# Optimization experiments

Measured on AMD Instinct MI355X. Metric: run time of the kernel, lower is better.

## Reference

```python
import jax, jax.numpy as jnp
import numpy as np

V, E, H, ENC, ATT = 10000, 256, 512, 512, 512
B, S, NF, MAXLEN = 128, 25, 196, 64


def setup_inputs() -> dict:
    key = jax.random.key(0)
    ks = jax.random.split(key, 24)
    g = lambda k, shp: (jax.random.normal(k, shp, dtype=jnp.float32) * 0.05)
    emb = g(ks[0], (V, E)).at[0].set(0.0)  # padding_idx=0 row zeroed
    return {
        'decoder_input': jax.random.randint(ks[1], (B, S), 0, V, dtype=jnp.int32),
        'encoder_outputs': jax.random.normal(ks[2], (B, NF, ENC), dtype=jnp.float32),
        'emb': emb,
        'pos_emb': g(ks[3], (MAXLEN, E)),
        'Uw': g(ks[4], (ATT, ENC)), 'Ub': g(ks[5], (ATT,)),
        'Ww': g(ks[6], (ATT, H)), 'Wb': g(ks[7], (ATT,)),
        'Aw': g(ks[8], (1, ATT)), 'Ab': g(ks[9], (1,)),
        'init_h_w': g(ks[10], (H, ENC)), 'init_h_b': g(ks[11], (H,)),
        'init_c_w': g(ks[12], (H, ENC)), 'init_c_b': g(ks[13], (H,)),
        'W_ih': g(ks[14], (4 * H, E + ENC)), 'W_hh': g(ks[15], (4 * H, H)),
        'b_ih': g(ks[16], (4 * H,)), 'b_hh': g(ks[17], (4 * H,)),
        'fcn_w': g(ks[18], (V, H)), 'fcn_b': g(ks[19], (V,)),
    }


def reference(decoder_input, encoder_outputs, emb, pos_emb, Uw, Ub, Ww, Wb, Aw, Ab,
              init_h_w, init_h_b, init_c_w, init_c_b, W_ih, W_hh, b_ih, b_hh,
              fcn_w, fcn_b):
    # Loop-invariant attention key projection: U(features) -> [B, NF, ATT]
    u_hs = jnp.einsum('bne,ae->bna', encoder_outputs, Uw) + Ub
    mean_enc = encoder_outputs.mean(axis=1)                  # [B, ENC]
    h0 = mean_enc @ init_h_w.T + init_h_b                    # [B, H]
    c0 = mean_enc @ init_c_w.T + init_c_b
    tokens = decoder_input.T                                 # [S, B]
    positions = jnp.arange(tokens.shape[0])

    def step(carry, inp):
        h, c = carry
        tok, pos = inp
        embeds = emb[tok] + pos_emb[pos]                     # [B, E]
        w_ah = h @ Ww.T + Wb                                 # [B, ATT]
        scores = jnp.tanh(u_hs + w_ah[:, None, :]) @ Aw[0] + Ab[0]  # [B, NF]
        alpha = jax.nn.softmax(scores, axis=1)
        context = jnp.einsum('bnd,bn->bd', encoder_outputs, alpha)  # [B, ENC]
        x = jnp.concatenate([embeds, context], axis=1)       # [B, E+ENC]
        gates = x @ W_ih.T + b_ih + h @ W_hh.T + b_hh        # [B, 4H]
        i, f, g_, o = jnp.split(gates, 4, axis=1)
        c_new = jax.nn.sigmoid(f) * c + jax.nn.sigmoid(i) * jnp.tanh(g_)
        h_new = jax.nn.sigmoid(o) * jnp.tanh(c_new)
        out = h_new @ fcn_w.T + fcn_b                        # [B, V] (dropout=eval identity)
        return (h_new, c_new), (out, alpha)

    _, (outs, alphas) = jax.lax.scan(step, (h0, c0), (tokens, positions))
    return outs.transpose(1, 0, 2), alphas.transpose(1, 0, 2)
```

## Files before the change

kernel.cpp:

```cpp
#include <hip/hip_runtime.h>

constexpr int B_ = 128, S_ = 25, NF_ = 196, ENC_ = 512, ATT_ = 512;
constexpr int H_ = 512, E_ = 256, V_ = 10000, G4_ = 2048;
constexpr int VPAD_ = 10112;

typedef __attribute__((ext_vector_type(8))) __bf16 bf16x8;
typedef __attribute__((ext_vector_type(4))) __bf16 bf16x4;
typedef __attribute__((ext_vector_type(4))) float f32x4;

__device__ __forceinline__ float bflo(unsigned u) {
    return __builtin_bit_cast(float, u << 16);
}
__device__ __forceinline__ float bfhi(unsigned u) {
    return __builtin_bit_cast(float, u & 0xffff0000u);
}
__device__ __forceinline__ float fast_tanhf(float x) {
    float e = __expf(2.f * x);
    return 1.f - 2.f * __fdividef(1.f, e + 1.f);
}
__device__ __forceinline__ float fast_sigf(float x) {
    return __fdividef(1.f, 1.f + __expf(-x));
}

__device__ __forceinline__ int gperm(int n) {
    int j = (n & 15) + ((n >> 6) << 4);
    int g = (n >> 4) & 3;
    return g * 512 + j;
}

__device__ __forceinline__ void gload16(const __bf16* src, __bf16* dst) {
    __builtin_amdgcn_global_load_lds(
        (const __attribute__((address_space(1))) unsigned*)src,
        (__attribute__((address_space(3))) unsigned*)dst, 16, 0, 0);
}

__global__ __launch_bounds__(256) void k_setup(
    const float* __restrict__ enc, __bf16* __restrict__ enc_bf,
    const float* __restrict__ Uw, __bf16* __restrict__ Uw_bf,
    const float* __restrict__ Ww, unsigned* __restrict__ W2,
    const float* __restrict__ W_ih, __bf16* __restrict__ WihE_r,
    const float* __restrict__ W_hh, __bf16* __restrict__ Wcat,
    const float* __restrict__ b_ih, const float* __restrict__ b_hh,
    float* __restrict__ bsum_r,
    const int* __restrict__ dec, const float* __restrict__ emb,
    const float* __restrict__ pose, __bf16* __restrict__ embeds_bf,
    const float* __restrict__ fcw, __bf16* __restrict__ fcw_bf) {
    __shared__ float Ts[32][65];
    int bid = blockIdx.x, t = threadIdx.x;

    if (bid < 12544) {
        int i = bid * 256 + t;
        if (i < 3211264) {
            float4 v = *(const float4*)&enc[(size_t)i * 4];
            bf16x4 o;
            o[0] = (__bf16)v.x; o[1] = (__bf16)v.y; o[2] = (__bf16)v.z; o[3] = (__bf16)v.w;
            *(bf16x4*)&enc_bf[(size_t)i * 4] = o;
        }
    } else if (bid < 12800) {
        int i = (bid - 12544) * 256 + t;
        float4 v = *(const float4*)&Uw[(size_t)i * 4];
        bf16x4 o;
        o[0] = (__bf16)v.x; o[1] = (__bf16)v.y; o[2] = (__bf16)v.z; o[3] = (__bf16)v.w;
        *(bf16x4*)&Uw_bf[(size_t)i * 4] = o;
    } else if (bid < 12928) {
        int l = bid - 12800;
        int k0 = (l & 15) * 32, j0 = (l >> 4) * 64;
        int c = t & 31, rr = t >> 5;
#pragma unroll
        for (int i = 0; i < 8; ++i) {
            int j = j0 + rr + i * 8;
            Ts[c][rr + i * 8] = Ww[(size_t)j * 512 + k0 + c];
        }
        __syncthreads();
#pragma unroll
        for (int i = 0; i < 4; ++i) {
            int kr = (t >> 5) + i * 8;
            int jc = t & 31;
            __bf16 b0 = (__bf16)Ts[kr][2 * jc], b1 = (__bf16)Ts[kr][2 * jc + 1];
            unsigned u = (unsigned)__builtin_bit_cast(unsigned short, b0)
                       | ((unsigned)__builtin_bit_cast(unsigned short, b1) << 16);
            W2[(size_t)(k0 + kr) * 256 + (j0 >> 1) + jc] = u;
        }
    } else if (bid < 14976) {
        int n = bid - 12928;
        int row = gperm(n);
        WihE_r[(size_t)n * 256 + t] = (__bf16)W_ih[(size_t)row * 768 + t];
    } else if (bid < 17024) {
        int n = bid - 14976;
        int row = gperm(n);
#pragma unroll
        for (int i = 0; i < 4; ++i) {
            int k = t + i * 256;
            float v = (k < 512) ? W_ih[(size_t)row * 768 + 256 + k]
                                : W_hh[(size_t)row * 512 + (k - 512)];
            Wcat[(size_t)n * 1024 + k] = (__bf16)v;
        }
    } else if (bid < 17032) {
        int n = (bid - 17024) * 256 + t;
        int row = gperm(n);
        bsum_r[n] = b_ih[row] + b_hh[row];
    } else if (bid < 20232) {
        int bx = bid - 17032;
        int s = bx >> 7, b = bx & 127;
        int tok = dec[b * S_ + s];
        embeds_bf[(size_t)bx * E_ + t] = (__bf16)(emb[tok * E_ + t] + pose[s * E_ + t]);
    } else {
        int i = (bid - 20232) * 256 + t;
        if (i < VPAD_ * 512 / 4) {
            int e = i * 4;
            int row = e >> 9;
            bf16x4 o;
            if (row < V_) {
                float4 v = *(const float4*)&fcw[(size_t)row * 512 + (e & 511)];
                o[0] = (__bf16)v.x; o[1] = (__bf16)v.y; o[2] = (__bf16)v.z; o[3] = (__bf16)v.w;
            } else {
                o[0] = o[1] = o[2] = o[3] = (__bf16)0.f;
            }
            *(bf16x4*)&fcw_bf[(size_t)e] = o;
        }
    }
}

__global__ __launch_bounds__(1024) void k_init2(const float* __restrict__ enc,
                                                const float* __restrict__ ihw, const float* __restrict__ ihb,
                                                const float* __restrict__ icw, const float* __restrict__ icb,
                                                __bf16* __restrict__ Abuf0, float* __restrict__ cbuf) {
    __shared__ float pm[1024];
    __shared__ __align__(16) float mean[512];
    int b = blockIdx.x, t = threadIdx.x;
    int d = t & 511, q = t >> 9;
    const float* ep = enc + ((size_t)b * 196 + q * 98) * 512 + d;
    float sum = 0.f;
#pragma unroll 7
    for (int n = 0; n < 98; ++n) sum += ep[(size_t)n * 512];
    pm[t] = sum;
    __syncthreads();
    if (t < 512) mean[t] = (pm[t] + pm[t + 512]) * (1.f / 196.f);
    __syncthreads();
    int w = t >> 6, ln = t & 63;
    float4 m4a = *(const float4*)&mean[ln * 8];
    float4 m4b = *(const float4*)&mean[ln * 8 + 4];
#pragma unroll 4
    for (int i = 0; i < 32; ++i) {
        int j = i * 16 + w;
        const float4* wh = (const float4*)&ihw[(size_t)j * 512 + ln * 8];
        const float4* wc = (const float4*)&icw[(size_t)j * 512 + ln * 8];
        float4 ha = wh[0], hb = wh[1], ca = wc[0], cb = wc[1];
        float ah = m4a.x * ha.x + m4a.y * ha.y + m4a.z * ha.z + m4a.w * ha.w
                 + m4b.x * hb.x + m4b.y * hb.y + m4b.z * hb.z + m4b.w * hb.w;
        float ac = m4a.x * ca.x + m4a.y * ca.y + m4a.z * ca.z + m4a.w * ca.w
                 + m4b.x * cb.x + m4b.y * cb.y + m4b.z * cb.z + m4b.w * cb.w;
#pragma unroll
        for (int off = 32; off; off >>= 1) {
            ah += __shfl_xor(ah, off);
            ac += __shfl_xor(ac, off);
        }
        if (ln == 0) {
            Abuf0[(size_t)b * 1024 + 512 + j] = (__bf16)(ah + ihb[j]);
            cbuf[b * 512 + j] = ac + icb[j];
        }
    }
}

__global__ __launch_bounds__(256) void k_gemms(
    const __bf16* __restrict__ Aa, const __bf16* __restrict__ Ba,
    const float* __restrict__ ba, __bf16* __restrict__ Ca,
    const __bf16* __restrict__ Ab, const __bf16* __restrict__ Bb,
    const float* __restrict__ bb, __bf16* __restrict__ Cb) {
    __shared__ __align__(16) __bf16 As[128 * 64];
    __shared__ __align__(16) __bf16 Bs[128 * 64];
    int bid = blockIdx.x, tid = threadIdx.x;
    const __bf16 *A, *Bm;
    const float* bias;
    __bf16* C;
    int lda, K, ldc, m0, n0;
    if (bid < 784) {
        A = Aa; Bm = Ba; bias = ba; C = Ca; lda = 512; K = 512; ldc = 512;
        m0 = (bid % 196) * 128; n0 = (bid / 196) * 128;
    } else {
        int i = bid - 784;
        A = Ab; Bm = Bb; bias = bb; C = Cb; lda = 256; K = 256; ldc = 2048;
        m0 = (i % 25) * 128; n0 = (i / 25) * 128;
    }
    int lane = tid & 63, w = tid >> 6;
    int wm = (w & 1) * 64, wn = (w >> 1) * 64;
    f32x4 acc[4][4] = {};
    int lrow = lane >> 3;
    int kgd = lane & 7;

    for (int k0 = 0; k0 < K; k0 += 64) {
#pragma unroll
        for (int i = 0; i < 4; ++i) {
            int row = w * 32 + i * 8 + lrow;
            int kgs = kgd ^ (row & 7);
            gload16(A + (size_t)(m0 + row) * lda + k0 + kgs * 8, &As[row * 64 + kgd * 8]);
            gload16(Bm + (size_t)(n0 + row) * K + k0 + kgs * 8, &Bs[row * 64 + kgd * 8]);
        }
        __syncthreads();
        bf16x8 af[4][2], bfr[4][2];
#pragma unroll
        for (int f = 0; f < 4; ++f) {
#pragma unroll
            for (int ks = 0; ks < 2; ++ks) {
                int ra = wm + f * 16 + (lane & 15);
                int rb = wn + f * 16 + (lane & 15);
                int kgl = ks * 4 + (lane >> 4);
                af[f][ks]  = *(const bf16x8*)&As[ra * 64 + (kgl ^ (ra & 7)) * 8];
                bfr[f][ks] = *(const bf16x8*)&Bs[rb * 64 + (kgl ^ (rb & 7)) * 8];
            }
        }
#pragma unroll
        for (int fm = 0; fm < 4; ++fm)
#pragma unroll
            for (int fn = 0; fn < 4; ++fn)
#pragma unroll
                for (int ks = 0; ks < 2; ++ks)
                    acc[fm][fn] = __builtin_amdgcn_mfma_f32_16x16x32_bf16(
                        af[fm][ks], bfr[fn][ks], acc[fm][fn], 0, 0, 0);
        __syncthreads();
    }
    int cm = (lane >> 4) * 4, cn = lane & 15;
#pragma unroll
    for (int fm = 0; fm < 4; ++fm)
#pragma unroll
        for (int fn = 0; fn < 4; ++fn)
#pragma unroll
            for (int r = 0; r < 4; ++r) {
                int gm = m0 + wm + fm * 16 + cm + r;
                int gn = n0 + wn + fn * 16 + cn;
                C[(size_t)gm * ldc + gn] = (__bf16)(acc[fm][fn][r] + bias[gn]);
            }
}

__global__ __launch_bounds__(256) void k_fcn(
    const __bf16* __restrict__ A, const __bf16* __restrict__ Bm,
    const float* __restrict__ bias1, float* __restrict__ Cout) {
    __shared__ __align__(16) __bf16 As[128 * 64];
    __shared__ __align__(16) __bf16 Bs[128 * 64];
    int tid = threadIdx.x;
    int lane = tid & 63, w = tid >> 6;
    int nwg = gridDim.x * gridDim.y;
    int bid = blockIdx.y * gridDim.x + blockIdx.x;
    int q = nwg >> 3, r0 = nwg & 7;
    int xcd = bid & 7, lid = bid >> 3;
    int wgid = (xcd < r0) ? xcd * (q + 1) + lid : r0 * (q + 1) + (xcd - r0) * q + lid;
    int m0 = (wgid % gridDim.x) * 128;
    int n0 = (wgid / gridDim.x) * 128;

    int wm = (w & 1) * 64, wn = (w >> 1) * 64;
    f32x4 acc[4][4] = {};
    int lrow = lane >> 3;
    int kgd = lane & 7;

    for (int k0 = 0; k0 < 512; k0 += 64) {
#pragma unroll
        for (int i = 0; i < 4; ++i) {
            int row = w * 32 + i * 8 + lrow;
            int kgs = kgd ^ (row & 7);
            gload16(A + (size_t)(m0 + row) * 512 + k0 + kgs * 8, &As[row * 64 + kgd * 8]);
            gload16(Bm + (size_t)(n0 + row) * 512 + k0 + kgs * 8, &Bs[row * 64 + kgd * 8]);
        }
        __syncthreads();
        bf16x8 af[4][2], bfr[4][2];
#pragma unroll
        for (int f = 0; f < 4; ++f) {
#pragma unroll
            for (int ks = 0; ks < 2; ++ks) {
                int ra = wm + f * 16 + (lane & 15);
                int rb = wn + f * 16 + (lane & 15);
                int kgl = ks * 4 + (lane >> 4);
                af[f][ks]  = *(const bf16x8*)&As[ra * 64 + (kgl ^ (ra & 7)) * 8];
                bfr[f][ks] = *(const bf16x8*)&Bs[rb * 64 + (kgl ^ (rb & 7)) * 8];
            }
        }
#pragma unroll
        for (int fm = 0; fm < 4; ++fm)
#pragma unroll
            for (int fn = 0; fn < 4; ++fn)
#pragma unroll
                for (int ks = 0; ks < 2; ++ks)
                    acc[fm][fn] = __builtin_amdgcn_mfma_f32_16x16x32_bf16(
                        af[fm][ks], bfr[fn][ks], acc[fm][fn], 0, 0, 0);
        __syncthreads();
    }
    int cm = (lane >> 4) * 4, cn = lane & 15;
#pragma unroll
    for (int fm = 0; fm < 4; ++fm) {
#pragma unroll
        for (int fn = 0; fn < 4; ++fn) {
#pragma unroll
            for (int r = 0; r < 4; ++r) {
                int gm = m0 + wm + fm * 16 + cm + r;
                int gn = n0 + wn + fn * 16 + cn;
                if (gn < V_) {
                    int orow = (gm & 127) * S_ + (gm >> 7);
                    Cout[(size_t)orow * V_ + gn] = acc[fm][fn][r] + bias1[gn];
                }
            }
        }
    }
}

__global__ __launch_bounds__(1024) void k_attn2(
    const __bf16* __restrict__ u_hs,
    const unsigned* __restrict__ enc2,
    const unsigned* __restrict__ W2,
    const float* __restrict__ Wb, const float* __restrict__ Aw,
    __bf16* __restrict__ Abuf,
    float* __restrict__ alphas, int s) {
    __shared__ __align__(16) float hs[512];
    __shared__ float wah[512];
    __shared__ float pc[2048];
    __shared__ float sc[200];
    int b = blockIdx.x, t = threadIdx.x;
    int ln = t & 63, w = t >> 6;

    if (t < 256) {
        unsigned u = ((const unsigned*)Abuf)[b * 512 + 256 + t];
        hs[2 * t] = bflo(u); hs[2 * t + 1] = bfhi(u);
    }
    __syncthreads();
    {
        int jp = t & 255, kq = t >> 8;
        float a0 = 0.f, a1 = 0.f;
        const unsigned* wp = W2 + (size_t)(kq * 128) * 256 + jp;
        const float4* h4 = (const float4*)(hs + kq * 128);
#pragma unroll 4
        for (int k4 = 0; k4 < 32; ++k4) {
            float4 hk = h4[k4];
            unsigned w0 = wp[(k4 * 4 + 0) * 256];
            unsigned w1 = wp[(k4 * 4 + 1) * 256];
            unsigned w2 = wp[(k4 * 4 + 2) * 256];
            unsigned w3 = wp[(k4 * 4 + 3) * 256];
            a0 += hk.x * bflo(w0); a1 += hk.x * bfhi(w0);
            a0 += hk.y * bflo(w1); a1 += hk.y * bfhi(w1);
            a0 += hk.z * bflo(w2); a1 += hk.z * bfhi(w2);
            a0 += hk.w * bflo(w3); a1 += hk.w * bfhi(w3);
        }
        pc[kq * 512 + 2 * jp] = a0;
        pc[kq * 512 + 2 * jp + 1] = a1;
    }
    __syncthreads();
    if (t < 512)
        wah[t] = pc[t] + pc[512 + t] + pc[1024 + t] + pc[1536 + t] + Wb[t];
    __syncthreads();
    {
        float av[8], wv[8];
#pragma unroll
        for (int i = 0; i < 8; ++i) { av[i] = Aw[ln * 8 + i]; wv[i] = wah[ln * 8 + i]; }
        for (int n = w; n < NF_; n += 16) {
            bf16x8 u8 = *(const bf16x8*)(u_hs + ((size_t)(b * NF_ + n)) * 512 + ln * 8);
            float acc = 0.f;
#pragma unroll
            for (int i = 0; i < 8; ++i)
                acc += fast_tanhf((float)u8[i] + wv[i]) * av[i];
#pragma unroll
            for (int off = 32; off; off >>= 1) acc += __shfl_xor(acc, off);
            if (ln == 0) sc[n] = __expf(acc);
        }
    }
    __syncthreads();
    float sum = sc[ln] + sc[ln + 64] + sc[ln + 128];
    if (ln < 4) sum += sc[ln + 192];
#pragma unroll
    for (int off = 32; off; off >>= 1) sum += __shfl_xor(sum, off);
    float inv = __fdividef(1.f, sum);
    if (t < NF_) alphas[((size_t)b * S_ + s) * NF_ + t] = sc[t] * inv;
    {
        int p2 = t & 255, q2 = t >> 8;
        float c0 = 0.f, c1 = 0.f;
        for (int i = q2; i < NF_; i += 4) {
            unsigned u = enc2[((size_t)(b * NF_ + i)) * 256 + p2];
            float a = sc[i];
            c0 += a * bflo(u); c1 += a * bfhi(u);
        }
        pc[q2 * 512 + 2 * p2] = c0;
        pc[q2 * 512 + 2 * p2 + 1] = c1;
    }
    __syncthreads();
    if (t < 512)
        Abuf[(size_t)b * 1024 + t] =
            (__bf16)((pc[t] + pc[512 + t] + pc[1024 + t] + pc[1536 + t]) * inv);
}

__global__ __launch_bounds__(256) void k_gates(
    const __bf16* __restrict__ Abuf,
    const __bf16* __restrict__ Wcat,
    const __bf16* __restrict__ gatespre,
    float* __restrict__ cbuf,
    __bf16* __restrict__ AbufN,
    __bf16* __restrict__ Hall_bf,
    int s) {
    __shared__ __align__(16) __bf16 As[2][16 * 64];
    __shared__ __align__(16) __bf16 Bs[2][64 * 64];
    __shared__ float Red[1024];
    __shared__ float Gs[16][68];
    int t = threadIdx.x;
    int lane = t & 63, w = t >> 6;
    int m0 = blockIdx.x * 16, n0 = blockIdx.y * 64;
    int kh = w >> 1, nh = w & 1;
    f32x4 acc[2] = {};
    int ah = t >> 7;
    int arow = (t & 127) >> 3;
    int ake = (t & 7) * 8;
    int akg = t & 7;
    int srow = t >> 3;
    int ke = (t & 7) * 8;
    int kgw = t & 7;

    for (int k0 = 0; k0 < 512; k0 += 64) {
        {
            int kb = ah * 512 + k0;
            bf16x8 av = *(const bf16x8*)(Abuf + (size_t)(m0 + arow) * 1024 + kb + ake);
            *(bf16x8*)&As[ah][arow * 64 + (akg ^ (arow & 7)) * 8] = av;
        }
#pragma unroll
        for (int h = 0; h < 2; ++h) {
            int kb = h * 512 + k0;
#pragma unroll
            for (int it = 0; it < 2; ++it) {
                int row = it * 32 + srow;
                bf16x8 bv = *(const bf16x8*)(Wcat + (size_t)(n0 + row) * 1024 + kb + ke);
                *(bf16x8*)&Bs[h][row * 64 + (kgw ^ (row & 7)) * 8] = bv;
            }
        }
        __syncthreads();
        bf16x8 af[2], bfr[2][2];
#pragma unroll
        for (int ks = 0; ks < 2; ++ks) {
            int ra = lane & 15;
            int kgl = ks * 4 + (lane >> 4);
            af[ks] = *(const bf16x8*)&As[kh][ra * 64 + ((kgl ^ (ra & 7))) * 8];
#pragma unroll
            for (int fn = 0; fn < 2; ++fn) {
                int rb = nh * 32 + fn * 16 + (lane & 15);
                bfr[fn][ks] = *(const bf16x8*)&Bs[kh][rb * 64 + ((kgl ^ (rb & 7))) * 8];
            }
        }
#pragma unroll
        for (int fn = 0; fn < 2; ++fn)
#pragma unroll
            for (int ks = 0; ks < 2; ++ks)
                acc[fn] = __builtin_amdgcn_mfma_f32_16x16x32_bf16(
                    af[ks], bfr[fn][ks], acc[fn], 0, 0, 0);
        __syncthreads();
    }
    int base = (nh * 64 + lane) * 8;
    if (kh == 1) {
#pragma unroll
        for (int fn = 0; fn < 2; ++fn)
#pragma unroll
            for (int r = 0; r < 4; ++r) Red[base + fn * 4 + r] = acc[fn][r];
    }
    __syncthreads();
    if (kh == 0) {
        int cm = (lane >> 4) * 4, cn = lane & 15;
#pragma unroll
        for (int fn = 0; fn < 2; ++fn)
#pragma unroll
            for (int r = 0; r < 4; ++r)
                Gs[cm + r][nh * 32 + fn * 16 + cn] = acc[fn][r] + Red[base + fn * 4 + r];
    }
    __syncthreads();
    {
        int row = t >> 4, jlo = t & 15;
        int b = m0 + row;
        int j = (n0 >> 6) * 16 + jlo;
        const __bf16* gp = gatespre + ((size_t)(s * B_ + b)) * G4_ + n0 + jlo;
        float qi = Gs[row][jlo]      + (float)gp[0];
        float qf = Gs[row][16 + jlo] + (float)gp[16];
        float qg = Gs[row][32 + jlo] + (float)gp[32];
        float qo = Gs[row][48 + jlo] + (float)gp[48];
        float ig = fast_sigf(qi), fg = fast_sigf(qf);
        float gg = fast_tanhf(qg), og = fast_sigf(qo);
        int ci = b * 512 + j;
        float cnew = fg * cbuf[ci] + ig * gg;
        float hn = og * fast_tanhf(cnew);
        cbuf[ci] = cnew;
        __bf16 hb = (__bf16)hn;
        AbufN[(size_t)b * 1024 + 512 + j] = hb;
        Hall_bf[(size_t)(s + 1) * 65536 + ci] = hb;
    }
}

extern "C" void kernel_launch(void* const* d_in, const int* in_sizes, int n_in,
                              void* d_out, int out_size, void* d_ws, size_t ws_size,
                              hipStream_t stream) {
    const int*   dec  = (const int*)d_in[0];
    const float* enc  = (const float*)d_in[1];
    const float* emb  = (const float*)d_in[2];
    const float* pose = (const float*)d_in[3];
    const float* Uw   = (const float*)d_in[4];
    const float* Ub   = (const float*)d_in[5];
    const float* Ww   = (const float*)d_in[6];
    const float* Wb   = (const float*)d_in[7];
    const float* Aw   = (const float*)d_in[8];
    const float* ihw  = (const float*)d_in[10];
    const float* ihb  = (const float*)d_in[11];
    const float* icw  = (const float*)d_in[12];
    const float* icb  = (const float*)d_in[13];
    const float* W_ih = (const float*)d_in[14];
    const float* W_hh = (const float*)d_in[15];
    const float* b_ih = (const float*)d_in[16];
    const float* b_hh = (const float*)d_in[17];
    const float* fcw  = (const float*)d_in[18];
    const float* fcb  = (const float*)d_in[19];
    float* out = (float*)d_out;
    char*  wsb = (char*)d_ws;

    size_t o = 0;
    __bf16*   enc_bf   = (__bf16*)(wsb + o); o += (size_t)25088 * 512 * 2;
    __bf16*   u_hs_bf  = (__bf16*)(wsb + o); o += (size_t)25088 * 512 * 2;
    __bf16*   gpre_bf  = (__bf16*)(wsb + o); o += (size_t)3200 * 2048 * 2;
    __bf16*   Hall_bf  = (__bf16*)(wsb + o); o += (size_t)26 * 65536 * 2;
    float*    cbuf     = (float*)(wsb + o);  o += (size_t)65536 * 4;
    __bf16*   Abuf     = (__bf16*)(wsb + o); o += (size_t)2 * 128 * 1024 * 2;
    __bf16*   Uw_bf    = (__bf16*)(wsb + o); o += (size_t)262144 * 2;
    unsigned* W2       = (unsigned*)(wsb + o); o += (size_t)512 * 256 * 4;
    __bf16*   WihE_r   = (__bf16*)(wsb + o); o += (size_t)2048 * 256 * 2;
    __bf16*   embeds_bf= (__bf16*)(wsb + o); o += (size_t)3200 * 256 * 2;
    __bf16*   Wcat     = (__bf16*)(wsb + o); o += (size_t)2048 * 1024 * 2;
    float*    bsum_r   = (float*)(wsb + o);  o += (size_t)2048 * 4;
    __bf16*   fcw_bf   = (__bf16*)(wsb + o); o += (size_t)VPAD_ * 512 * 2;

    k_setup<<<25288, 256, 0, stream>>>(enc, enc_bf, Uw, Uw_bf, Ww, W2,
                                       W_ih, WihE_r, W_hh, Wcat,
                                       b_ih, b_hh, bsum_r,
                                       dec, emb, pose, embeds_bf, fcw, fcw_bf);
    k_init2<<<B_, 1024, 0, stream>>>(enc, ihw, ihb, icw, icb, Abuf, cbuf);
    k_gemms<<<1184, 256, 0, stream>>>(enc_bf, Uw_bf, Ub, u_hs_bf,
                                      embeds_bf, WihE_r, bsum_r, gpre_bf);

    for (int s = 0; s < S_; ++s) {
        __bf16* Ap = Abuf + (size_t)(s & 1) * 131072;
        __bf16* An = Abuf + (size_t)((s + 1) & 1) * 131072;
        k_attn2<<<B_, 1024, 0, stream>>>(u_hs_bf, (const unsigned*)enc_bf, W2, Wb, Aw,
                                         Ap, out + 32000000, s);
        k_gates<<<dim3(8, 32), 256, 0, stream>>>(Ap, Wcat, gpre_bf, cbuf, An, Hall_bf, s);
    }

    k_fcn<<<dim3(25, 79), 256, 0, stream>>>(Hall_bf + 65536, fcw_bf, fcb, out);
}
```

Before: 1.335 ms.

## Split attention over feature halves and move softmax normalization into gates kernel

The per-step attention kernel now runs on a 128x2 grid of 512-thread blocks. Each block handles half of the 196 features and writes unnormalized context partials, exp-score sums and raw exp scores to workspace. The gates kernel combines the two halves, normalizes by the summed denominator while loading its A tile, and writes the alphas. This gives the attention step twice as many blocks to spread across CUs, but each block now recomputes the full W·h projection and extra global traffic passes between the kernels.

```diff
diff --git a/kernel.cpp b/kernel.cpp
--- a/kernel.cpp
+++ b/kernel.cpp
@@ -301,18 +301,20 @@
     }
 }
 
-__global__ __launch_bounds__(1024) void k_attn2(
+__global__ __launch_bounds__(512) void k_attn3(
     const __bf16* __restrict__ u_hs,
     const unsigned* __restrict__ enc2,
     const unsigned* __restrict__ W2,
     const float* __restrict__ Wb, const float* __restrict__ Aw,
-    __bf16* __restrict__ Abuf,
-    float* __restrict__ alphas, int s) {
+    const __bf16* __restrict__ Abuf,
+    float* __restrict__ pctx,
+    float* __restrict__ lpart,
+    float* __restrict__ esg) {
     __shared__ __align__(16) float hs[512];
     __shared__ float wah[512];
-    __shared__ float pc[2048];
-    __shared__ float sc[200];
-    int b = blockIdx.x, t = threadIdx.x;
+    __shared__ float pc[1024];
+    __shared__ float es[100];
+    int b = blockIdx.x, hh = blockIdx.y, t = threadIdx.x;
     int ln = t & 63, w = t >> 6;
 
     if (t < 256) {
@@ -321,12 +323,12 @@
     }
     __syncthreads();
     {
-        int jp = t & 255, kq = t >> 8;
+        int jp = t & 255, q = t >> 8;
         float a0 = 0.f, a1 = 0.f;
-        const unsigned* wp = W2 + (size_t)(kq * 128) * 256 + jp;
-        const float4* h4 = (const float4*)(hs + kq * 128);
+        const unsigned* wp = W2 + (size_t)(q * 256) * 256 + jp;
+        const float4* h4 = (const float4*)(hs + q * 256);
 #pragma unroll 4
-        for (int k4 = 0; k4 < 32; ++k4) {
+        for (int k4 = 0; k4 < 64; ++k4) {
             float4 hk = h4[k4];
             unsigned w0 = wp[(k4 * 4 + 0) * 256];
             unsigned w1 = wp[(k4 * 4 + 1) * 256];
@@ -337,18 +339,18 @@
             a0 += hk.z * bflo(w2); a1 += hk.z * bfhi(w2);
             a0 += hk.w * bflo(w3); a1 += hk.w * bfhi(w3);
         }
-        pc[kq * 512 + 2 * jp] = a0;
-        pc[kq * 512 + 2 * jp + 1] = a1;
-    }
-    __syncthreads();
-    if (t < 512)
-        wah[t] = pc[t] + pc[512 + t] + pc[1024 + t] + pc[1536 + t] + Wb[t];
+        pc[q * 512 + 2 * jp] = a0;
+        pc[q * 512 + 2 * jp + 1] = a1;
+    }
+    __syncthreads();
+    wah[t] = pc[t] + pc[512 + t] + Wb[t];
     __syncthreads();
     {
         float av[8], wv[8];
 #pragma unroll
         for (int i = 0; i < 8; ++i) { av[i] = Aw[ln * 8 + i]; wv[i] = wah[ln * 8 + i]; }
-        for (int n = w; n < NF_; n += 16) {
+        for (int nl = w; nl < 98; nl += 8) {
+            int n = hh * 98 + nl;
             bf16x8 u8 = *(const bf16x8*)(u_hs + ((size_t)(b * NF_ + n)) * 512 + ln * 8);
             float acc = 0.f;
 #pragma unroll
@@ -356,31 +358,30 @@
                 acc += fast_tanhf((float)u8[i] + wv[i]) * av[i];
 #pragma unroll
             for (int off = 32; off; off >>= 1) acc += __shfl_xor(acc, off);
-            if (ln == 0) sc[n] = __expf(acc);
-        }
-    }
-    __syncthreads();
-    float sum = sc[ln] + sc[ln + 64] + sc[ln + 128];
-    if (ln < 4) sum += sc[ln + 192];
-#pragma unroll
-    for (int off = 32; off; off >>= 1) sum += __shfl_xor(sum, off);
-    float inv = __fdividef(1.f, sum);
-    if (t < NF_) alphas[((size_t)b * S_ + s) * NF_ + t] = sc[t] * inv;
+            if (ln == 0) es[nl] = __expf(acc);
+        }
+    }
+    __syncthreads();
     {
         int p2 = t & 255, q2 = t >> 8;
         float c0 = 0.f, c1 = 0.f;
-        for (int i = q2; i < NF_; i += 4) {
-            unsigned u = enc2[((size_t)(b * NF_ + i)) * 256 + p2];
-            float a = sc[i];
+        for (int i = q2; i < 98; i += 2) {
+            unsigned u = enc2[((size_t)(b * NF_ + hh * 98 + i)) * 256 + p2];
+            float a = es[i];
             c0 += a * bflo(u); c1 += a * bfhi(u);
         }
         pc[q2 * 512 + 2 * p2] = c0;
         pc[q2 * 512 + 2 * p2 + 1] = c1;
     }
     __syncthreads();
-    if (t < 512)
-        Abuf[(size_t)b * 1024 + t] =
-            (__bf16)((pc[t] + pc[512 + t] + pc[1024 + t] + pc[1536 + t]) * inv);
+    pctx[((size_t)(hh * 128 + b)) * 512 + t] = pc[t] + pc[512 + t];
+    if (t < 98) esg[b * 256 + hh * 98 + t] = es[t];
+    if (t < 64) {
+        float v = es[t] + ((t + 64 < 98) ? es[t + 64] : 0.f);
+#pragma unroll
+        for (int off = 32; off; off >>= 1) v += __shfl_xor(v, off);
+        if (t == 0) lpart[hh * 128 + b] = v;
+    }
 }
 
 __global__ __launch_bounds__(256) void k_gates(
@@ -390,7 +391,8 @@
     float* __restrict__ cbuf,
     __bf16* __restrict__ AbufN,
     __bf16* __restrict__ Hall_bf,
-    int s) {
+    const float* __restrict__ pctx, const float* __restrict__ lpart,
+    const float* __restrict__ esg, float* __restrict__ alphas, int s) {
     __shared__ __align__(16) __bf16 As[2][16 * 64];
     __shared__ __align__(16) __bf16 Bs[2][64 * 64];
     __shared__ float Red[1024];
@@ -408,11 +410,35 @@
     int ke = (t & 7) * 8;
     int kgw = t & 7;
 
+    if (blockIdx.y == 0) {
+        for (int qq = t; qq < 16 * 196; qq += 256) {
+            int row = qq / 196, n = qq - row * 196;
+            float inv = __fdividef(1.f, lpart[m0 + row] + lpart[128 + m0 + row]);
+            alphas[((size_t)(m0 + row) * S_ + s) * NF_ + n] =
+                esg[(m0 + row) * 256 + n] * inv;
+        }
+    }
+
     for (int k0 = 0; k0 < 512; k0 += 64) {
-        {
-            int kb = ah * 512 + k0;
-            bf16x8 av = *(const bf16x8*)(Abuf + (size_t)(m0 + arow) * 1024 + kb + ake);
-            *(bf16x8*)&As[ah][arow * 64 + (akg ^ (arow & 7)) * 8] = av;
+        if (ah == 0) {
+            const float* p0 = pctx + (size_t)(m0 + arow) * 512 + k0 + ake;
+            const float* p1 = p0 + 128 * 512;
+            float inv = __fdividef(1.f, lpart[m0 + arow] + lpart[128 + m0 + arow]);
+            float4 a0v = *(const float4*)p0, a1v = *(const float4*)(p0 + 4);
+            float4 b0v = *(const float4*)p1, b1v = *(const float4*)(p1 + 4);
+            bf16x8 v;
+            v[0] = (__bf16)((a0v.x + b0v.x) * inv);
+            v[1] = (__bf16)((a0v.y + b0v.y) * inv);
+            v[2] = (__bf16)((a0v.z + b0v.z) * inv);
+            v[3] = (__bf16)((a0v.w + b0v.w) * inv);
+            v[4] = (__bf16)((a1v.x + b1v.x) * inv);
+            v[5] = (__bf16)((a1v.y + b1v.y) * inv);
+            v[6] = (__bf16)((a1v.z + b1v.z) * inv);
+            v[7] = (__bf16)((a1v.w + b1v.w) * inv);
+            *(bf16x8*)&As[0][arow * 64 + (akg ^ (arow & 7)) * 8] = v;
+        } else {
+            bf16x8 av = *(const bf16x8*)(Abuf + (size_t)(m0 + arow) * 1024 + 512 + k0 + ake);
+            *(bf16x8*)&As[1][arow * 64 + (akg ^ (arow & 7)) * 8] = av;
         }
 #pragma unroll
         for (int h = 0; h < 2; ++h) {
@@ -522,6 +548,9 @@
     __bf16*   Wcat     = (__bf16*)(wsb + o); o += (size_t)2048 * 1024 * 2;
     float*    bsum_r   = (float*)(wsb + o);  o += (size_t)2048 * 4;
     __bf16*   fcw_bf   = (__bf16*)(wsb + o); o += (size_t)VPAD_ * 512 * 2;
+    float*    pctx     = (float*)(wsb + o);  o += (size_t)2 * 128 * 512 * 4;
+    float*    lpart    = (float*)(wsb + o);  o += (size_t)256 * 4;
+    float*    esg      = (float*)(wsb + o);  o += (size_t)128 * 256 * 4;
 
     k_setup<<<25288, 256, 0, stream>>>(enc, enc_bf, Uw, Uw_bf, Ww, W2,
                                        W_ih, WihE_r, W_hh, Wcat,
@@ -534,9 +563,10 @@
     for (int s = 0; s < S_; ++s) {
         __bf16* Ap = Abuf + (size_t)(s & 1) * 131072;
         __bf16* An = Abuf + (size_t)((s + 1) & 1) * 131072;
-        k_attn2<<<B_, 1024, 0, stream>>>(u_hs_bf, (const unsigned*)enc_bf, W2, Wb, Aw,
-                                         Ap, out + 32000000, s);
-        k_gates<<<dim3(8, 32), 256, 0, stream>>>(Ap, Wcat, gpre_bf, cbuf, An, Hall_bf, s);
+        k_attn3<<<dim3(B_, 2), 512, 0, stream>>>(u_hs_bf, (const unsigned*)enc_bf, W2,
+                                                 Wb, Aw, Ap, pctx, lpart, esg);
+        k_gates<<<dim3(8, 32), 256, 0, stream>>>(Ap, Wcat, gpre_bf, cbuf, An, Hall_bf,
+                                                 pctx, lpart, esg, out + 32000000, s);
     }
 
     k_fcn<<<dim3(25, 79), 256, 0, stream>>>(Hall_bf + 65536, fcw_bf, fcb, out);
```

Result: slower. 1.383 ms (+3.6%).

## Fuse attention and gate kernels per step using flag-based inter-block sync

Applied to the files above, without the earlier changes.

Merges the per-step attention kernel and the LSTM gate GEMM kernel into one launch of 384 blocks. The first 128 blocks compute attention per batch row and publish a per-row flag with release semantics. The remaining blocks spin on the flags for their 16-row slab before running the gate MFMA GEMM. This removes one kernel launch and its boundary per step (25 fewer launches) and lets gate tiles start as soon as their rows are ready. The risks are deadlock if the spinning blocks get scheduled ahead of the attention blocks and occupy the resources they need, and wasted occupancy because the gate blocks launch with 1024 threads but use only 256.

```diff
diff --git a/kernel.cpp b/kernel.cpp
--- a/kernel.cpp
+++ b/kernel.cpp
@@ -44,7 +44,8 @@
     float* __restrict__ bsum_r,
     const int* __restrict__ dec, const float* __restrict__ emb,
     const float* __restrict__ pose, __bf16* __restrict__ embeds_bf,
-    const float* __restrict__ fcw, __bf16* __restrict__ fcw_bf) {
+    const float* __restrict__ fcw, __bf16* __restrict__ fcw_bf,
+    int* __restrict__ flag) {
     __shared__ float Ts[32][65];
     int bid = blockIdx.x, t = threadIdx.x;
 
@@ -104,7 +105,7 @@
         int s = bx >> 7, b = bx & 127;
         int tok = dec[b * S_ + s];
         embeds_bf[(size_t)bx * E_ + t] = (__bf16)(emb[tok * E_ + t] + pose[s * E_ + t]);
-    } else {
+    } else if (bid < 25288) {
         int i = (bid - 20232) * 256 + t;
         if (i < VPAD_ * 512 / 4) {
             int e = i * 4;
@@ -118,6 +119,8 @@
             }
             *(bf16x4*)&fcw_bf[(size_t)e] = o;
         }
+    } else {
+        if (t < 128) flag[t] = 0;
     }
 }
 
@@ -301,185 +304,199 @@
     }
 }
 
-__global__ __launch_bounds__(1024) void k_attn2(
-    const __bf16* __restrict__ u_hs,
-    const unsigned* __restrict__ enc2,
-    const unsigned* __restrict__ W2,
-    const float* __restrict__ Wb, const float* __restrict__ Aw,
-    __bf16* __restrict__ Abuf,
-    float* __restrict__ alphas, int s) {
+__global__ __launch_bounds__(1024) void k_step(
+    const __bf16* __restrict__ u_hs, const unsigned* __restrict__ enc2,
+    const unsigned* __restrict__ W2, const float* __restrict__ Wb,
+    const float* __restrict__ Aw, const __bf16* __restrict__ Wcat,
+    const __bf16* __restrict__ gatespre, float* __restrict__ cbuf,
+    __bf16* __restrict__ Abuf, __bf16* __restrict__ AbufN,
+    __bf16* __restrict__ Hall_bf, float* __restrict__ alphas,
+    int* __restrict__ flag, int s) {
     __shared__ __align__(16) float hs[512];
     __shared__ float wah[512];
     __shared__ float pc[2048];
     __shared__ float sc[200];
-    int b = blockIdx.x, t = threadIdx.x;
-    int ln = t & 63, w = t >> 6;
-
-    if (t < 256) {
-        unsigned u = ((const unsigned*)Abuf)[b * 512 + 256 + t];
-        hs[2 * t] = bflo(u); hs[2 * t + 1] = bfhi(u);
-    }
-    __syncthreads();
-    {
-        int jp = t & 255, kq = t >> 8;
-        float a0 = 0.f, a1 = 0.f;
-        const unsigned* wp = W2 + (size_t)(kq * 128) * 256 + jp;
-        const float4* h4 = (const float4*)(hs + kq * 128);
-#pragma unroll 4
-        for (int k4 = 0; k4 < 32; ++k4) {
-            float4 hk = h4[k4];
-            unsigned w0 = wp[(k4 * 4 + 0) * 256];
-            unsigned w1 = wp[(k4 * 4 + 1) * 256];
-            unsigned w2 = wp[(k4 * 4 + 2) * 256];
-            unsigned w3 = wp[(k4 * 4 + 3) * 256];
-            a0 += hk.x * bflo(w0); a1 += hk.x * bfhi(w0);
-            a0 += hk.y * bflo(w1); a1 += hk.y * bfhi(w1);
-            a0 += hk.z * bflo(w2); a1 += hk.z * bfhi(w2);
-            a0 += hk.w * bflo(w3); a1 += hk.w * bfhi(w3);
-        }
-        pc[kq * 512 + 2 * jp] = a0;
-        pc[kq * 512 + 2 * jp + 1] = a1;
-    }
-    __syncthreads();
-    if (t < 512)
-        wah[t] = pc[t] + pc[512 + t] + pc[1024 + t] + pc[1536 + t] + Wb[t];
-    __syncthreads();
-    {
-        float av[8], wv[8];
-#pragma unroll
-        for (int i = 0; i < 8; ++i) { av[i] = Aw[ln * 8 + i]; wv[i] = wah[ln * 8 + i]; }
-        for (int n = w; n < NF_; n += 16) {
-            bf16x8 u8 = *(const bf16x8*)(u_hs + ((size_t)(b * NF_ + n)) * 512 + ln * 8);
-            float acc = 0.f;
-#pragma unroll
-            for (int i = 0; i < 8; ++i)
-                acc += fast_tanhf((float)u8[i] + wv[i]) * av[i];
-#pragma unroll
-            for (int off = 32; off; off >>= 1) acc += __shfl_xor(acc, off);
-            if (ln == 0) sc[n] = __expf(acc);
-        }
-    }
-    __syncthreads();
-    float sum = sc[ln] + sc[ln + 64] + sc[ln + 128];
-    if (ln < 4) sum += sc[ln + 192];
-#pragma unroll
-    for (int off = 32; off; off >>= 1) sum += __shfl_xor(sum, off);
-    float inv = __fdividef(1.f, sum);
-    if (t < NF_) alphas[((size_t)b * S_ + s) * NF_ + t] = sc[t] * inv;
-    {
-        int p2 = t & 255, q2 = t >> 8;
-        float c0 = 0.f, c1 = 0.f;
-        for (int i = q2; i < NF_; i += 4) {
-            unsigned u = enc2[((size_t)(b * NF_ + i)) * 256 + p2];
-            float a = sc[i];
-            c0 += a * bflo(u); c1 += a * bfhi(u);
-        }
-        pc[q2 * 512 + 2 * p2] = c0;
-        pc[q2 * 512 + 2 * p2 + 1] = c1;
-    }
-    __syncthreads();
-    if (t < 512)
-        Abuf[(size_t)b * 1024 + t] =
-            (__bf16)((pc[t] + pc[512 + t] + pc[1024 + t] + pc[1536 + t]) * inv);
-}
-
-__global__ __launch_bounds__(256) void k_gates(
-    const __bf16* __restrict__ Abuf,
-    const __bf16* __restrict__ Wcat,
-    const __bf16* __restrict__ gatespre,
-    float* __restrict__ cbuf,
-    __bf16* __restrict__ AbufN,
-    __bf16* __restrict__ Hall_bf,
-    int s) {
-    __shared__ __align__(16) __bf16 As[2][16 * 64];
-    __shared__ __align__(16) __bf16 Bs[2][64 * 64];
+    __shared__ __align__(16) __bf16 Asg[2][16 * 64];
+    __shared__ __align__(16) __bf16 Bsg[2][64 * 64];
     __shared__ float Red[1024];
     __shared__ float Gs[16][68];
-    int t = threadIdx.x;
-    int lane = t & 63, w = t >> 6;
-    int m0 = blockIdx.x * 16, n0 = blockIdx.y * 64;
-    int kh = w >> 1, nh = w & 1;
-    f32x4 acc[2] = {};
-    int ah = t >> 7;
-    int arow = (t & 127) >> 3;
-    int ake = (t & 7) * 8;
-    int akg = t & 7;
-    int srow = t >> 3;
-    int ke = (t & 7) * 8;
-    int kgw = t & 7;
-
-    for (int k0 = 0; k0 < 512; k0 += 64) {
+
+    int bid = blockIdx.x, t = threadIdx.x;
+
+    if (bid < 128) {
+        int b = bid;
+        int ln = t & 63, w = t >> 6;
+        if (t < 256) {
+            unsigned u = ((const unsigned*)Abuf)[b * 512 + 256 + t];
+            hs[2 * t] = bflo(u); hs[2 * t + 1] = bfhi(u);
+        }
+        __syncthreads();
         {
-            int kb = ah * 512 + k0;
-            bf16x8 av = *(const bf16x8*)(Abuf + (size_t)(m0 + arow) * 1024 + kb + ake);
-            *(bf16x8*)&As[ah][arow * 64 + (akg ^ (arow & 7)) * 8] = av;
-        }
-#pragma unroll
-        for (int h = 0; h < 2; ++h) {
-            int kb = h * 512 + k0;
-#pragma unroll
-            for (int it = 0; it < 2; ++it) {
-                int row = it * 32 + srow;
-                bf16x8 bv = *(const bf16x8*)(Wcat + (size_t)(n0 + row) * 1024 + kb + ke);
-                *(bf16x8*)&Bs[h][row * 64 + (kgw ^ (row & 7)) * 8] = bv;
-            }
-        }
-        __syncthreads();
-        bf16x8 af[2], bfr[2][2];
-#pragma unroll
-        for (int ks = 0; ks < 2; ++ks) {
-            int ra = lane & 15;
-            int kgl = ks * 4 + (lane >> 4);
-            af[ks] = *(const bf16x8*)&As[kh][ra * 64 + ((kgl ^ (ra & 7))) * 8];
-#pragma unroll
-            for (int fn = 0; fn < 2; ++fn) {
-                int rb = nh * 32 + fn * 16 + (lane & 15);
-                bfr[fn][ks] = *(const bf16x8*)&Bs[kh][rb * 64 + ((kgl ^ (rb & 7))) * 8];
-            }
-        }
-#pragma unroll
-        for (int fn = 0; fn < 2; ++fn)
-#pragma unroll
-            for (int ks = 0; ks < 2; ++ks)
-                acc[fn] = __builtin_amdgcn_mfma_f32_16x16x32_bf16(
-                    af[ks], bfr[fn][ks], acc[fn], 0, 0, 0);
-        __syncthreads();
-    }
-    int base = (nh * 64 + lane) * 8;
-    if (kh == 1) {
-#pragma unroll
-        for (int fn = 0; fn < 2; ++fn)
-#pragma unroll
-            for (int r = 0; r < 4; ++r) Red[base + fn * 4 + r] = acc[fn][r];
-    }
-    __syncthreads();
-    if (kh == 0) {
-        int cm = (lane >> 4) * 4, cn = lane & 15;
-#pragma unroll
-        for (int fn = 0; fn < 2; ++fn)
-#pragma unroll
-            for (int r = 0; r < 4; ++r)
-                Gs[cm + r][nh * 32 + fn * 16 + cn] = acc[fn][r] + Red[base + fn * 4 + r];
-    }
-    __syncthreads();
-    {
-        int row = t >> 4, jlo = t & 15;
-        int b = m0 + row;
-        int j = (n0 >> 6) * 16 + jlo;
-        const __bf16* gp = gatespre + ((size_t)(s * B_ + b)) * G4_ + n0 + jlo;
-        float qi = Gs[row][jlo]      + (float)gp[0];
-        float qf = Gs[row][16 + jlo] + (float)gp[16];
-        float qg = Gs[row][32 + jlo] + (float)gp[32];
-        float qo = Gs[row][48 + jlo] + (float)gp[48];
-        float ig = fast_sigf(qi), fg = fast_sigf(qf);
-        float gg = fast_tanhf(qg), og = fast_sigf(qo);
-        int ci = b * 512 + j;
-        float cnew = fg * cbuf[ci] + ig * gg;
-        float hn = og * fast_tanhf(cnew);
-        cbuf[ci] = cnew;
-        __bf16 hb = (__bf16)hn;
-        AbufN[(size_t)b * 1024 + 512 + j] = hb;
-        Hall_bf[(size_t)(s + 1) * 65536 + ci] = hb;
+            int jp = t & 255, kq = t >> 8;
+            float a0 = 0.f, a1 = 0.f;
+            const unsigned* wp = W2 + (size_t)(kq * 128) * 256 + jp;
+            const float4* h4 = (const float4*)(hs + kq * 128);
+#pragma unroll 4
+            for (int k4 = 0; k4 < 32; ++k4) {
+                float4 hk = h4[k4];
+                unsigned w0 = wp[(k4 * 4 + 0) * 256];
+                unsigned w1 = wp[(k4 * 4 + 1) * 256];
+                unsigned w2 = wp[(k4 * 4 + 2) * 256];
+                unsigned w3 = wp[(k4 * 4 + 3) * 256];
+                a0 += hk.x * bflo(w0); a1 += hk.x * bfhi(w0);
+                a0 += hk.y * bflo(w1); a1 += hk.y * bfhi(w1);
+                a0 += hk.z * bflo(w2); a1 += hk.z * bfhi(w2);
+                a0 += hk.w * bflo(w3); a1 += hk.w * bfhi(w3);
+            }
+            pc[kq * 512 + 2 * jp] = a0;
+            pc[kq * 512 + 2 * jp + 1] = a1;
+        }
+        __syncthreads();
+        if (t < 512)
+            wah[t] = pc[t] + pc[512 + t] + pc[1024 + t] + pc[1536 + t] + Wb[t];
+        __syncthreads();
+        {
+            float av[8], wv[8];
+#pragma unroll
+            for (int i = 0; i < 8; ++i) { av[i] = Aw[ln * 8 + i]; wv[i] = wah[ln * 8 + i]; }
+            for (int n = w; n < NF_; n += 16) {
+                bf16x8 u8 = *(const bf16x8*)(u_hs + ((size_t)(b * NF_ + n)) * 512 + ln * 8);
+                float acc = 0.f;
+#pragma unroll
+                for (int i = 0; i < 8; ++i)
+                    acc += fast_tanhf((float)u8[i] + wv[i]) * av[i];
+#pragma unroll
+                for (int off = 32; off; off >>= 1) acc += __shfl_xor(acc, off);
+                if (ln == 0) sc[n] = __expf(acc);
+            }
+        }
+        __syncthreads();
+        float sum = sc[ln] + sc[ln + 64] + sc[ln + 128];
+        if (ln < 4) sum += sc[ln + 192];
+#pragma unroll
+        for (int off = 32; off; off >>= 1) sum += __shfl_xor(sum, off);
+        float inv = __fdividef(1.f, sum);
+        if (t < NF_) alphas[((size_t)b * S_ + s) * NF_ + t] = sc[t] * inv;
+        {
+            int p2 = t & 255, q2 = t >> 8;
+            float c0 = 0.f, c1 = 0.f;
+            for (int i = q2; i < NF_; i += 4) {
+                unsigned u = enc2[((size_t)(b * NF_ + i)) * 256 + p2];
+                float a = sc[i];
+                c0 += a * bflo(u); c1 += a * bfhi(u);
+            }
+            pc[q2 * 512 + 2 * p2] = c0;
+            pc[q2 * 512 + 2 * p2 + 1] = c1;
+        }
+        __syncthreads();
+        if (t < 512)
+            Abuf[(size_t)b * 1024 + t] =
+                (__bf16)((pc[t] + pc[512 + t] + pc[1024 + t] + pc[1536 + t]) * inv);
+        __syncthreads();
+        if (t == 0) {
+            __threadfence();
+            __hip_atomic_store(&flag[b], s + 1, __ATOMIC_RELEASE, __HIP_MEMORY_SCOPE_AGENT);
+        }
+    } else {
+        if (t >= 256) return;
+        int gbk = bid - 128;
+        int m0 = (gbk & 7) * 16, n0 = (gbk >> 3) * 64;
+        if (t < 64) {
+            for (;;) {
+                int v = (t < 16)
+                    ? __hip_atomic_load(&flag[m0 + t], __ATOMIC_RELAXED, __HIP_MEMORY_SCOPE_AGENT)
+                    : 0x7fffffff;
+                if (__all(v >= s + 1)) break;
+                __builtin_amdgcn_s_sleep(32);
+            }
+            __threadfence();
+        }
+        __syncthreads();
+
+        int lane = t & 63, w = t >> 6;
+        int kh = w >> 1, nh = w & 1;
+        f32x4 acc[2] = {};
+        int ah = t >> 7;
+        int arow = (t & 127) >> 3;
+        int ake = (t & 7) * 8;
+        int akg = t & 7;
+        int srow = t >> 3;
+        int ke = (t & 7) * 8;
+        int kgw = t & 7;
+
+        for (int k0 = 0; k0 < 512; k0 += 64) {
+            {
+                int kb = ah * 512 + k0;
+                bf16x8 av = *(const bf16x8*)(Abuf + (size_t)(m0 + arow) * 1024 + kb + ake);
+                *(bf16x8*)&Asg[ah][arow * 64 + (akg ^ (arow & 7)) * 8] = av;
+            }
+#pragma unroll
+            for (int h = 0; h < 2; ++h) {
+                int kb = h * 512 + k0;
+#pragma unroll
+                for (int it = 0; it < 2; ++it) {
+                    int row = it * 32 + srow;
+                    bf16x8 bv = *(const bf16x8*)(Wcat + (size_t)(n0 + row) * 1024 + kb + ke);
+                    *(bf16x8*)&Bsg[h][row * 64 + (kgw ^ (row & 7)) * 8] = bv;
+                }
+            }
+            __syncthreads();
+            bf16x8 af[2], bfr[2][2];
+#pragma unroll
+            for (int ks = 0; ks < 2; ++ks) {
+                int ra = lane & 15;
+                int kgl = ks * 4 + (lane >> 4);
+                af[ks] = *(const bf16x8*)&Asg[kh][ra * 64 + ((kgl ^ (ra & 7))) * 8];
+#pragma unroll
+                for (int fn = 0; fn < 2; ++fn) {
+                    int rb = nh * 32 + fn * 16 + (lane & 15);
+                    bfr[fn][ks] = *(const bf16x8*)&Bsg[kh][rb * 64 + ((kgl ^ (rb & 7))) * 8];
+                }
+            }
+#pragma unroll
+            for (int fn = 0; fn < 2; ++fn)
+#pragma unroll
+                for (int ks = 0; ks < 2; ++ks)
+                    acc[fn] = __builtin_amdgcn_mfma_f32_16x16x32_bf16(
+                        af[ks], bfr[fn][ks], acc[fn], 0, 0, 0);
+            __syncthreads();
+        }
+        int base = (nh * 64 + lane) * 8;
+        if (kh == 1) {
+#pragma unroll
+            for (int fn = 0; fn < 2; ++fn)
+#pragma unroll
+                for (int r = 0; r < 4; ++r) Red[base + fn * 4 + r] = acc[fn][r];
+        }
+        __syncthreads();
+        if (kh == 0) {
+            int cm = (lane >> 4) * 4, cn = lane & 15;
+#pragma unroll
+            for (int fn = 0; fn < 2; ++fn)
+#pragma unroll
+                for (int r = 0; r < 4; ++r)
+                    Gs[cm + r][nh * 32 + fn * 16 + cn] = acc[fn][r] + Red[base + fn * 4 + r];
+        }
+        __syncthreads();
+        {
+            int row = t >> 4, jlo = t & 15;
+            int b = m0 + row;
+            int j = (n0 >> 6) * 16 + jlo;
+            const __bf16* gp = gatespre + ((size_t)(s * B_ + b)) * G4_ + n0 + jlo;
+            float qi = Gs[row][jlo]      + (float)gp[0];
+            float qf = Gs[row][16 + jlo] + (float)gp[16];
+            float qg = Gs[row][32 + jlo] + (float)gp[32];
+            float qo = Gs[row][48 + jlo] + (float)gp[48];
+            float ig = fast_sigf(qi), fg = fast_sigf(qf);
+            float gg = fast_tanhf(qg), og = fast_sigf(qo);
+            int ci = b * 512 + j;
+            float cnew = fg * cbuf[ci] + ig * gg;
+            float hn = og * fast_tanhf(cnew);
+            cbuf[ci] = cnew;
+            __bf16 hb = (__bf16)hn;
+            AbufN[(size_t)b * 1024 + 512 + j] = hb;
+            Hall_bf[(size_t)(s + 1) * 65536 + ci] = hb;
+        }
     }
 }
 
@@ -522,11 +539,12 @@
     __bf16*   Wcat     = (__bf16*)(wsb + o); o += (size_t)2048 * 1024 * 2;
     float*    bsum_r   = (float*)(wsb + o);  o += (size_t)2048 * 4;
     __bf16*   fcw_bf   = (__bf16*)(wsb + o); o += (size_t)VPAD_ * 512 * 2;
-
-    k_setup<<<25288, 256, 0, stream>>>(enc, enc_bf, Uw, Uw_bf, Ww, W2,
+    int*      flags    = (int*)(wsb + o);    o += 128 * 4;
+
+    k_setup<<<25289, 256, 0, stream>>>(enc, enc_bf, Uw, Uw_bf, Ww, W2,
                                        W_ih, WihE_r, W_hh, Wcat,
                                        b_ih, b_hh, bsum_r,
-                                       dec, emb, pose, embeds_bf, fcw, fcw_bf);
+                                       dec, emb, pose, embeds_bf, fcw, fcw_bf, flags);
     k_init2<<<B_, 1024, 0, stream>>>(enc, ihw, ihb, icw, icb, Abuf, cbuf);
     k_gemms<<<1184, 256, 0, stream>>>(enc_bf, Uw_bf, Ub, u_hs_bf,
                                       embeds_bf, WihE_r, bsum_r, gpre_bf);
@@ -534,9 +552,9 @@
     for (int s = 0; s < S_; ++s) {
         __bf16* Ap = Abuf + (size_t)(s & 1) * 131072;
         __bf16* An = Abuf + (size_t)((s + 1) & 1) * 131072;
-        k_attn2<<<B_, 1024, 0, stream>>>(u_hs_bf, (const unsigned*)enc_bf, W2, Wb, Aw,
-                                         Ap, out + 32000000, s);
-        k_gates<<<dim3(8, 32), 256, 0, stream>>>(Ap, Wcat, gpre_bf, cbuf, An, Hall_bf, s);
+        k_step<<<384, 1024, 0, stream>>>(u_hs_bf, (const unsigned*)enc_bf, W2, Wb, Aw,
+                                         Wcat, gpre_bf, cbuf, Ap, An, Hall_bf,
+                                         out + 32000000, flags, s);
     }
 
     k_fcn<<<dim3(25, 79), 256, 0, stream>>>(Hall_bf + 65536, fcw_bf, fcb, out);
```

Result: slower. 1.566 ms (+17.3%).
